# Optimization experiments

Hardware: AMD Instinct MI355X
Metric: run time of the kernel (lower is better)

Reference implementation:

```python
import jax, jax.numpy as jnp
import numpy as np
import math

EMBED_DIM = 1024
NUM_HEADS = 16
HEAD_DIM = EMBED_DIM // NUM_HEADS
ROPE_BASE = 10000.0


def _rope_cache(seq_len, dim, dtype=jnp.float32):
    inv_freq = 1.0 / (ROPE_BASE ** (jnp.arange(0, dim, 2, dtype=jnp.float32) / dim))
    t = jnp.arange(seq_len, dtype=jnp.float32)
    freqs = t[:, None] * inv_freq[None, :]          # [S, D/2]
    emb = jnp.concatenate([freqs, freqs], axis=-1)  # [S, D]
    return jnp.cos(emb).astype(dtype), jnp.sin(emb).astype(dtype)


def _rotate_half(x):
    x1, x2 = jnp.split(x, 2, axis=-1)
    return jnp.concatenate([-x2, x1], axis=-1)


def setup_inputs() -> dict:
    key = jax.random.key(0)
    ks = jax.random.split(key, 12)
    B, S, E = 2, 2048, EMBED_DIM
    s = 1.0 / math.sqrt(E)
    inp = {
        "query": jax.random.normal(ks[0], (B, S, E), jnp.float32),
        "key": jax.random.normal(ks[1], (B, S, E), jnp.float32),
        "value": jax.random.normal(ks[2], (B, S, E), jnp.float32),
        "Wq": jax.random.normal(ks[3], (E, E), jnp.float32) * s,
        "bq": jnp.zeros((E,), jnp.float32),
        "Wk": jax.random.normal(ks[4], (E, E), jnp.float32) * s,
        "bk": jnp.zeros((E,), jnp.float32),
        "Wv": jax.random.normal(ks[5], (E, E), jnp.float32) * s,
        "bv": jnp.zeros((E,), jnp.float32),
        "Wo": jax.random.normal(ks[6], (E, E), jnp.float32) * s,
        "bo": jnp.zeros((E,), jnp.float32),
    }
    return inp


def reference(query, key, value, Wq, bq, Wk, bk, Wv, bv, Wo, bo):
    B, S, E = query.shape
    H, D = NUM_HEADS, HEAD_DIM

    def proj(x, W, b):  # torch Linear: x @ W.T + b -> [B,H,S,D]
        return (x @ W.T + b).reshape(B, -1, H, D).transpose(0, 2, 1, 3)

    q = proj(query, Wq, bq)
    k = proj(key, Wk, bk)
    v = proj(value, Wv, bv)

    cos, sin = _rope_cache(S, D, q.dtype)  # [S, D]
    cos = cos[None, None]                  # [1,1,S,D]
    sin = sin[None, None]
    q = q * cos + _rotate_half(q) * sin
    k = k * cos + _rotate_half(k) * sin

    scale = 1.0 / math.sqrt(D)
    scores = jnp.einsum("bhsd,bhtd->bhst", q, k) * scale  # [B,H,S,S]
    causal = jnp.triu(jnp.ones((S, S), bool), k=1)
    scores = jnp.where(causal[None, None], -jnp.inf, scores)
    attn = jax.nn.softmax(scores, axis=-1)
    out = jnp.einsum("bhst,bhtd->bhsd", attn, v)           # [B,H,S,D]
    out = out.transpose(0, 2, 1, 3).reshape(B, S, E)
    return out @ Wo.T + bo
```

## Files before the change

kernel.cpp:

```cpp
#include <hip/hip_runtime.h>
#include <math.h>

typedef unsigned short u16;
typedef __attribute__((ext_vector_type(4))) float f32x4;
typedef __attribute__((ext_vector_type(8))) short bf16x8;

#define SEQ   2048
#define EMB   1024
#define NH    16
#define HD    64
#define MROWS 4096

__device__ __forceinline__ u16 f2b(float f) {
    unsigned u = __float_as_uint(f);
    u += 0x7fff + ((u >> 16) & 1);
    return (u16)(u >> 16);
}
__device__ __forceinline__ unsigned pack_bf16x2(float a, float b) {
    unsigned ua = __float_as_uint(a) + 0x8000u;
    unsigned ub = __float_as_uint(b) + 0x8000u;
    return __builtin_amdgcn_perm(ub, ua, 0x07060302u);
}
__device__ __forceinline__ void gld16(const u16* g, const u16* l) {
    __builtin_amdgcn_global_load_lds((const __attribute__((address_space(1))) void*)g,
                                     (__attribute__((address_space(3))) void*)l, 16, 0, 0);
}

__global__ void k_f2b3(const float* __restrict__ s0, const float* __restrict__ s1,
                       const float* __restrict__ s2, u16* d0, u16* d1, u16* d2, int n8) {
    const float* src = (blockIdx.z == 0) ? s0 : (blockIdx.z == 1 ? s1 : s2);
    u16* dst = (blockIdx.z == 0) ? d0 : (blockIdx.z == 1 ? d1 : d2);
    int i = blockIdx.x * blockDim.x + threadIdx.x;
    if (i >= n8) return;
    const float4* s4 = (const float4*)src;
    float4 a = s4[i * 2], b = s4[i * 2 + 1];
    union { u16 u[8]; uint4 v; } o;
    o.u[0] = f2b(a.x); o.u[1] = f2b(a.y); o.u[2] = f2b(a.z); o.u[3] = f2b(a.w);
    o.u[4] = f2b(b.x); o.u[5] = f2b(b.y); o.u[6] = f2b(b.z); o.u[7] = f2b(b.w);
    ((uint4*)dst)[i] = o.v;
}
__global__ void k_f2b4(const float* __restrict__ s0, const float* __restrict__ s1,
                       const float* __restrict__ s2, const float* __restrict__ s3,
                       u16* d0, u16* d1, u16* d2, u16* d3, int n8) {
    const float* src = (blockIdx.z == 0) ? s0 : (blockIdx.z == 1 ? s1 : (blockIdx.z == 2 ? s2 : s3));
    u16* dst = (blockIdx.z == 0) ? d0 : (blockIdx.z == 1 ? d1 : (blockIdx.z == 2 ? d2 : d3));
    int i = blockIdx.x * blockDim.x + threadIdx.x;
    if (i >= n8) return;
    const float4* s4 = (const float4*)src;
    float4 a = s4[i * 2], b = s4[i * 2 + 1];
    union { u16 u[8]; uint4 v; } o;
    o.u[0] = f2b(a.x); o.u[1] = f2b(a.y); o.u[2] = f2b(a.z); o.u[3] = f2b(a.w);
    o.u[4] = f2b(b.x); o.u[5] = f2b(b.y); o.u[6] = f2b(b.z); o.u[7] = f2b(b.w);
    ((uint4*)dst)[i] = o.v;
}

struct GemmArgs {
    const u16* A; const u16* Bw; const float* bias; u16* Cb; float* Cf;
};

__global__ __launch_bounds__(256) void k_gemm_bt(GemmArgs g0, GemmArgs g1, GemmArgs g2,
                                                 int K, int mode) {
    GemmArgs g = (blockIdx.z == 0) ? g0 : (blockIdx.z == 1 ? g1 : g2);
    __shared__ u16 sbuf[2][8192];

    int tid = threadIdx.x;
    int wave = tid >> 6, lane = tid & 63, quad = lane >> 4, l16 = lane & 15;
    int wm = wave >> 1, wn = wave & 1;
    int m0 = blockIdx.y * 128, n0 = blockIdx.x * 128;

    auto stage = [&](int k0, u16* buf) {
#pragma unroll
        for (int pp = 0; pp < 4; pp++) {
            int slot = pp * 256 + tid;
            int p = slot & 3;
            const u16* gsrc;
            if (pp < 2) {
                int row = slot >> 2;
                int c = p ^ (row & 3);
                gsrc = g.A + (size_t)(m0 + row) * K + k0 + c * 8;
            } else {
                int row = (slot >> 2) - 128;
                int c = p ^ (row & 3);
                gsrc = g.Bw + (size_t)(n0 + row) * K + k0 + c * 8;
            }
            gld16(gsrc, buf + slot * 8);
        }
    };

    f32x4 acc[4][4];
#pragma unroll
    for (int i = 0; i < 4; i++)
#pragma unroll
        for (int j = 0; j < 4; j++) acc[i][j] = (f32x4){0.f, 0.f, 0.f, 0.f};

    int nk = K >> 5;
    stage(0, sbuf[0]);
    for (int ks = 0; ks < nk; ks++) {
        __syncthreads();
        if (ks + 1 < nk) stage((ks + 1) << 5, sbuf[(ks + 1) & 1]);
        const u16* Ab = sbuf[ks & 1];
        const u16* Bb = Ab + 4096;
        bf16x8 af[4], bfr[4];
#pragma unroll
        for (int i = 0; i < 4; i++) {
            int row = wm * 64 + i * 16 + l16;
            af[i] = *(const bf16x8*)&Ab[row * 32 + (quad ^ (row & 3)) * 8];
        }
#pragma unroll
        for (int j = 0; j < 4; j++) {
            int row = wn * 64 + j * 16 + l16;
            bfr[j] = *(const bf16x8*)&Bb[row * 32 + (quad ^ (row & 3)) * 8];
        }
#pragma unroll
        for (int i = 0; i < 4; i++)
#pragma unroll
            for (int j = 0; j < 4; j++)
                acc[i][j] = __builtin_amdgcn_mfma_f32_16x16x32_bf16(af[i], bfr[j], acc[i][j], 0, 0, 0);
    }

    if (mode == 0) {
        if (blockIdx.z < 2) {
            float qscale = (blockIdx.z == 0) ? 0.18033688011112042f : 1.0f;
#pragma unroll
            for (int j = 0; j < 2; j++) {
                int col1 = n0 + wn * 64 + j * 16 + l16;
                int dd1 = col1 & 63;
                int h = col1 >> 6;
                float inv = __expf(-(float)dd1 * 0.28782313662425575f);
                float b1 = g.bias[col1], b2 = g.bias[col1 + 32];
#pragma unroll
                for (int i = 0; i < 4; i++)
#pragma unroll
                    for (int r = 0; r < 4; r++) {
                        int row = m0 + wm * 64 + i * 16 + quad * 4 + r;
                        int b = row >> 11, s = row & (SEQ - 1);
                        float sn, cs;
                        __sincosf((float)s * inv, &sn, &cs);
                        float x1 = acc[i][j][r] + b1;
                        float x2 = acc[i][j + 2][r] + b2;
                        size_t base = ((size_t)(b * NH + h) * SEQ + s) << 6;
                        g.Cb[base + dd1]      = f2b((x1 * cs - x2 * sn) * qscale);
                        g.Cb[base + dd1 + 32] = f2b((x2 * cs + x1 * sn) * qscale);
                    }
            }
        } else {
#pragma unroll
            for (int j = 0; j < 4; j++) {
                int col = n0 + wn * 64 + j * 16 + l16;
                float bv = g.bias[col];
                int h = col >> 6, dd = col & 63;
#pragma unroll
                for (int i = 0; i < 4; i++)
#pragma unroll
                    for (int r = 0; r < 4; r++) {
                        int row = m0 + wm * 64 + i * 16 + quad * 4 + r;
                        int b = row >> 11, s = row & (SEQ - 1);
                        g.Cb[((size_t)((b * NH + h) * HD) + dd) * SEQ + s] = f2b(acc[i][j][r] + bv);
                    }
            }
        }
    } else {
#pragma unroll
        for (int i = 0; i < 4; i++)
#pragma unroll
            for (int r = 0; r < 4; r++) {
                int row = m0 + wm * 64 + i * 16 + quad * 4 + r;
#pragma unroll
                for (int j = 0; j < 4; j++) {
                    int col = n0 + wn * 64 + j * 16 + l16;
                    g.Cf[(size_t)row * EMB + col] = acc[i][j][r] + g.bias[col];
                }
            }
    }
}

__global__ __launch_bounds__(256, 2) void k_attn(const u16* __restrict__ Q,
                                                 const u16* __restrict__ K,
                                                 const u16* __restrict__ Vt,
                                                 u16* __restrict__ O) {
    __shared__ u16 sbuf[2][8192];
    __shared__ u16 Pl[4][3072];
    int tid = threadIdx.x;
    int w = tid >> 6, lane = tid & 63, quad = lane >> 4, l16 = lane & 15;
    int bh = blockIdx.y;
    int qt = (blockIdx.y & 16) ? blockIdx.x : (15 - blockIdx.x);
    int q0w = qt * 128 + w * 32;

    const u16* Qb = Q + (size_t)bh * SEQ * HD;
    const u16* Kb = K + (size_t)bh * SEQ * HD;
    const u16* Vb = Vt + (size_t)bh * HD * SEQ;
    u16* pl = Pl[w];

    auto stage = [&](int t0, u16* buf) {
#pragma unroll
        for (int pp = 0; pp < 4; pp++) {
            int slot = pp * 256 + tid;
            int r = (slot >> 3) & 63;
            int p = slot & 7;
            int c = p ^ (r & 7);
            const u16* gsrc = (pp < 2) ? Kb + (size_t)(t0 + r) * HD + c * 8
                                       : Vb + (size_t)r * SEQ + t0 + c * 8;
            gld16(gsrc, buf + slot * 8);
        }
    };

    bf16x8 bq[2][2];
#pragma unroll
    for (int g = 0; g < 2; g++) {
        size_t base = (size_t)(q0w + g * 16 + l16) * HD + quad * 8;
        bq[g][0] = *(const bf16x8*)&Qb[base];
        bq[g][1] = *(const bf16x8*)&Qb[base + 32];
    }

    f32x4 o2[2][4];
#pragma unroll
    for (int g = 0; g < 2; g++)
#pragma unroll
        for (int jd = 0; jd < 4; jd++) o2[g][jd] = (f32x4){0.f, 0.f, 0.f, 0.f};
    float m_i[2] = {-INFINITY, -INFINITY};
    float l_p[2] = {0.f, 0.f};

    int niter = 2 * qt + 2;
    stage(0, sbuf[0]);
    for (int it = 0; it < niter; ++it) {
        __syncthreads();
        if (it + 1 < niter) stage((it + 1) * 64, sbuf[(it + 1) & 1]);
        const u16* Kl = sbuf[it & 1];
        const u16* Vl = Kl + 4096;
        int t0 = it * 64;

        bf16x8 kf[4][2], vf[4][2];
#pragma unroll
        for (int mt = 0; mt < 4; mt++) {
            int row = mt * 16 + l16;
            kf[mt][0] = *(const bf16x8*)&Kl[row * 64 + (quad ^ (row & 7)) * 8];
            kf[mt][1] = *(const bf16x8*)&Kl[row * 64 + ((quad + 4) ^ (row & 7)) * 8];
            vf[mt][0] = *(const bf16x8*)&Vl[row * 64 + (quad ^ (row & 7)) * 8];
            vf[mt][1] = *(const bf16x8*)&Vl[row * 64 + ((quad + 4) ^ (row & 7)) * 8];
        }

#pragma unroll
        for (int g = 0; g < 2; g++) {
            int qmin = q0w + g * 16;
            if (t0 > qmin + 15) continue;

            f32x4 sc[4];
#pragma unroll
            for (int mt = 0; mt < 4; mt++) {
                sc[mt] = (f32x4){0.f, 0.f, 0.f, 0.f};
                sc[mt] = __builtin_amdgcn_mfma_f32_16x16x32_bf16(kf[mt][0], bq[g][0], sc[mt], 0, 0, 0);
                sc[mt] = __builtin_amdgcn_mfma_f32_16x16x32_bf16(kf[mt][1], bq[g][1], sc[mt], 0, 0, 0);
            }

            if (t0 + 63 > qmin) {
                int q = qmin + l16;
#pragma unroll
                for (int mt = 0; mt < 4; mt++)
#pragma unroll
                    for (int r = 0; r < 4; r++) {
                        int t = t0 + mt * 16 + quad * 4 + r;
                        if (t > q) sc[mt][r] = -INFINITY;
                    }
            }

            float rm = -INFINITY;
#pragma unroll
            for (int mt = 0; mt < 4; mt++)
#pragma unroll
                for (int r = 0; r < 4; r++) rm = fmaxf(rm, sc[mt][r]);
            rm = fmaxf(rm, __shfl_xor(rm, 16, 64));
            rm = fmaxf(rm, __shfl_xor(rm, 32, 64));
            float mnew = fmaxf(m_i[g], rm);
            float al = __builtin_amdgcn_exp2f(m_i[g] - mnew);
            m_i[g] = mnew;

            float rs = 0.f;
#pragma unroll
            for (int mt = 0; mt < 4; mt++)
#pragma unroll
                for (int r = 0; r < 4; r++) {
                    float p = __builtin_amdgcn_exp2f(sc[mt][r] - mnew);
                    sc[mt][r] = p;
                    rs += p;
                }
            l_p[g] = l_p[g] * al + rs;

            u16* plg = pl + g * 1024;
#pragma unroll
            for (int mt = 0; mt < 4; mt++) {
                uint2 pk;
                pk.x = pack_bf16x2(sc[mt][0], sc[mt][1]);
                pk.y = pack_bf16x2(sc[mt][2], sc[mt][3]);
                int chunk = 2 * mt + (quad >> 1);
                *(uint2*)&plg[l16 * 64 + (chunk ^ (l16 & 7)) * 8 + (quad & 1) * 4] = pk;
            }

#pragma unroll
            for (int jd = 0; jd < 4; jd++)
#pragma unroll
                for (int r = 0; r < 4; r++) o2[g][jd][r] *= al;

            bf16x8 pb0 = *(const bf16x8*)&plg[l16 * 64 + (quad ^ (l16 & 7)) * 8];
            bf16x8 pb1 = *(const bf16x8*)&plg[l16 * 64 + ((quad + 4) ^ (l16 & 7)) * 8];

#pragma unroll
            for (int jd = 0; jd < 4; jd++) {
                o2[g][jd] = __builtin_amdgcn_mfma_f32_16x16x32_bf16(vf[jd][0], pb0, o2[g][jd], 0, 0, 0);
                o2[g][jd] = __builtin_amdgcn_mfma_f32_16x16x32_bf16(vf[jd][1], pb1, o2[g][jd], 0, 0, 0);
            }
        }
    }

    int b = bh >> 4, h = bh & (NH - 1);
#pragma unroll
    for (int g = 0; g < 2; g++) {
        float l = l_p[g];
        l += __shfl_xor(l, 16, 64);
        l += __shfl_xor(l, 32, 64);
        float inv = 1.f / l;
#pragma unroll
        for (int jd = 0; jd < 4; jd++) {
            uint2 pk;
            pk.x = pack_bf16x2(o2[g][jd][0] * inv, o2[g][jd][1] * inv);
            pk.y = pack_bf16x2(o2[g][jd][2] * inv, o2[g][jd][3] * inv);
            *(uint2*)&pl[l16 * 72 + jd * 16 + quad * 4] = pk;
        }
        int row = lane >> 2, dc = (lane & 3) * 16;
        uint4 d0 = *(const uint4*)&pl[row * 72 + dc];
        uint4 d1 = *(const uint4*)&pl[row * 72 + dc + 8];
        int q = q0w + g * 16 + row;
        size_t addr = (size_t)(b * SEQ + q) * EMB + h * HD + dc;
        *(uint4*)&O[addr] = d0;
        *(uint4*)&O[addr + 8] = d1;
    }
}

extern "C" void kernel_launch(void* const* d_in, const int* in_sizes, int n_in,
                              void* d_out, int out_size, void* d_ws, size_t ws_size,
                              hipStream_t stream) {
    const float* query = (const float*)d_in[0];
    const float* key_  = (const float*)d_in[1];
    const float* value = (const float*)d_in[2];
    const float* Wq = (const float*)d_in[3];
    const float* bq = (const float*)d_in[4];
    const float* Wk = (const float*)d_in[5];
    const float* bk = (const float*)d_in[6];
    const float* Wv = (const float*)d_in[7];
    const float* bv = (const float*)d_in[8];
    const float* Wo = (const float*)d_in[9];
    const float* bo = (const float*)d_in[10];
    float* out = (float*)d_out;

    char* ws = (char*)d_ws;
    const size_t MB = 1u << 20;
    u16* xq  = (u16*)(ws + 0 * MB);
    u16* xk  = (u16*)(ws + 8 * MB);
    u16* xv  = (u16*)(ws + 16 * MB);
    u16* wqb = (u16*)(ws + 24 * MB);
    u16* wkb = (u16*)(ws + 26 * MB);
    u16* wvb = (u16*)(ws + 28 * MB);
    u16* wob = (u16*)(ws + 30 * MB);
    u16* Qp  = (u16*)(ws + 32 * MB);
    u16* Kp  = (u16*)(ws + 40 * MB);
    u16* Vt  = (u16*)(ws + 48 * MB);
    u16* Ab  = xk;

    const int NX = MROWS * EMB;
    const int NW = EMB * EMB;

    k_f2b3<<<dim3(NX / (256 * 8), 1, 3), 256, 0, stream>>>(query, key_, value, xq, xk, xv, NX / 8);
    k_f2b4<<<dim3(NW / (256 * 8), 1, 4), 256, 0, stream>>>(Wq, Wk, Wv, Wo, wqb, wkb, wvb, wob, NW / 8);

    GemmArgs gq = { xq, wqb, bq, Qp, nullptr };
    GemmArgs gk = { xk, wkb, bk, Kp, nullptr };
    GemmArgs gv = { xv, wvb, bv, Vt, nullptr };
    k_gemm_bt<<<dim3(EMB / 128, MROWS / 128, 3), 256, 0, stream>>>(gq, gk, gv, EMB, 0);

    k_attn<<<dim3(16, 32), 256, 0, stream>>>(Qp, Kp, Vt, Ab);

    GemmArgs go = { Ab, wob, bo, nullptr, out };
    k_gemm_bt<<<dim3(EMB / 128, MROWS / 128, 1), 256, 0, stream>>>(go, go, go, EMB, 1);
}
```

Baseline: 242.5 us.

## Persistent attention scheduler, LDS-transposed V epilogue, smaller-tile output GEMM

Attention becomes a persistent kernel with 768 blocks that pull (head, query-tile) items from a global atomic counter, longest causal tiles first, for better load balance. The counter is zeroed by a new kernel and lives in the xv workspace buffer. The V projection epilogue now transposes through shared memory so it writes coalesced 16-byte stores instead of scattered 2-byte ones. The output projection gets its own 64x128-tile GEMM kernel to launch more blocks. Costs are an extra launch, an atomic per work item, and the loss of the launch_bounds occupancy hint on attention.

```diff
diff --git a/kernel.cpp b/kernel.cpp
--- a/kernel.cpp
+++ b/kernel.cpp
@@ -54,19 +54,24 @@
     ((uint4*)dst)[i] = o.v;
 }
 
+__global__ void k_zero(int* p) { if (threadIdx.x == 0) *p = 0; }
+
 struct GemmArgs {
-    const u16* A; const u16* Bw; const float* bias; u16* Cb; float* Cf;
+    const u16* A; const u16* Bw; const float* bias; u16* Cb;
 };
 
-__global__ __launch_bounds__(256) void k_gemm_bt(GemmArgs g0, GemmArgs g1, GemmArgs g2,
-                                                 int K, int mode) {
+__global__ __launch_bounds__(256) void k_gemm_qkv(GemmArgs g0, GemmArgs g1, GemmArgs g2) {
     GemmArgs g = (blockIdx.z == 0) ? g0 : (blockIdx.z == 1 ? g1 : g2);
-    __shared__ u16 sbuf[2][8192];
+    __shared__ union {
+        u16 s[2][8192];
+        u16 tr[4][4608];
+    } sh;
 
     int tid = threadIdx.x;
     int wave = tid >> 6, lane = tid & 63, quad = lane >> 4, l16 = lane & 15;
     int wm = wave >> 1, wn = wave & 1;
     int m0 = blockIdx.y * 128, n0 = blockIdx.x * 128;
+    const int K = EMB;
 
     auto stage = [&](int k0, u16* buf) {
 #pragma unroll
@@ -94,11 +99,11 @@
         for (int j = 0; j < 4; j++) acc[i][j] = (f32x4){0.f, 0.f, 0.f, 0.f};
 
     int nk = K >> 5;
-    stage(0, sbuf[0]);
+    stage(0, sh.s[0]);
     for (int ks = 0; ks < nk; ks++) {
         __syncthreads();
-        if (ks + 1 < nk) stage((ks + 1) << 5, sbuf[(ks + 1) & 1]);
-        const u16* Ab = sbuf[ks & 1];
+        if (ks + 1 < nk) stage((ks + 1) << 5, sh.s[(ks + 1) & 1]);
+        const u16* Ab = sh.s[ks & 1];
         const u16* Bb = Ab + 4096;
         bf16x8 af[4], bfr[4];
 #pragma unroll
@@ -118,220 +123,296 @@
                 acc[i][j] = __builtin_amdgcn_mfma_f32_16x16x32_bf16(af[i], bfr[j], acc[i][j], 0, 0, 0);
     }
 
-    if (mode == 0) {
-        if (blockIdx.z < 2) {
-            float qscale = (blockIdx.z == 0) ? 0.18033688011112042f : 1.0f;
-#pragma unroll
-            for (int j = 0; j < 2; j++) {
-                int col1 = n0 + wn * 64 + j * 16 + l16;
-                int dd1 = col1 & 63;
-                int h = col1 >> 6;
-                float inv = __expf(-(float)dd1 * 0.28782313662425575f);
-                float b1 = g.bias[col1], b2 = g.bias[col1 + 32];
-#pragma unroll
-                for (int i = 0; i < 4; i++)
-#pragma unroll
-                    for (int r = 0; r < 4; r++) {
-                        int row = m0 + wm * 64 + i * 16 + quad * 4 + r;
-                        int b = row >> 11, s = row & (SEQ - 1);
-                        float sn, cs;
-                        __sincosf((float)s * inv, &sn, &cs);
-                        float x1 = acc[i][j][r] + b1;
-                        float x2 = acc[i][j + 2][r] + b2;
-                        size_t base = ((size_t)(b * NH + h) * SEQ + s) << 6;
-                        g.Cb[base + dd1]      = f2b((x1 * cs - x2 * sn) * qscale);
-                        g.Cb[base + dd1 + 32] = f2b((x2 * cs + x1 * sn) * qscale);
-                    }
-            }
-        } else {
-#pragma unroll
-            for (int j = 0; j < 4; j++) {
-                int col = n0 + wn * 64 + j * 16 + l16;
-                float bv = g.bias[col];
-                int h = col >> 6, dd = col & 63;
-#pragma unroll
-                for (int i = 0; i < 4; i++)
-#pragma unroll
-                    for (int r = 0; r < 4; r++) {
-                        int row = m0 + wm * 64 + i * 16 + quad * 4 + r;
-                        int b = row >> 11, s = row & (SEQ - 1);
-                        g.Cb[((size_t)((b * NH + h) * HD) + dd) * SEQ + s] = f2b(acc[i][j][r] + bv);
-                    }
-            }
+    if (blockIdx.z < 2) {
+        float qscale = (blockIdx.z == 0) ? 0.18033688011112042f : 1.0f;
+#pragma unroll
+        for (int j = 0; j < 2; j++) {
+            int col1 = n0 + wn * 64 + j * 16 + l16;
+            int dd1 = col1 & 63;
+            int h = col1 >> 6;
+            float inv = __expf(-(float)dd1 * 0.28782313662425575f);
+            float b1 = g.bias[col1], b2 = g.bias[col1 + 32];
+#pragma unroll
+            for (int i = 0; i < 4; i++)
+#pragma unroll
+                for (int r = 0; r < 4; r++) {
+                    int row = m0 + wm * 64 + i * 16 + quad * 4 + r;
+                    int b = row >> 11, s = row & (SEQ - 1);
+                    float sn, cs;
+                    __sincosf((float)s * inv, &sn, &cs);
+                    float x1 = acc[i][j][r] + b1;
+                    float x2 = acc[i][j + 2][r] + b2;
+                    size_t base = ((size_t)(b * NH + h) * SEQ + s) << 6;
+                    g.Cb[base + dd1]      = f2b((x1 * cs - x2 * sn) * qscale);
+                    g.Cb[base + dd1 + 32] = f2b((x2 * cs + x1 * sn) * qscale);
+                }
         }
     } else {
-#pragma unroll
-        for (int i = 0; i < 4; i++)
-#pragma unroll
-            for (int r = 0; r < 4; r++) {
-                int row = m0 + wm * 64 + i * 16 + quad * 4 + r;
-#pragma unroll
-                for (int j = 0; j < 4; j++) {
-                    int col = n0 + wn * 64 + j * 16 + l16;
-                    g.Cf[(size_t)row * EMB + col] = acc[i][j][r] + g.bias[col];
-                }
-            }
+        __syncthreads();
+        u16* tr = sh.tr[wave];
+        int h = (n0 >> 6) + wn;
+        int b = m0 >> 11;
+        int s0 = (m0 & (SEQ - 1)) + wm * 64;
+#pragma unroll
+        for (int j = 0; j < 4; j++) {
+            float bv = g.bias[n0 + wn * 64 + j * 16 + l16];
+#pragma unroll
+            for (int i = 0; i < 4; i++) {
+                uint2 pk;
+                pk.x = pack_bf16x2(acc[i][j][0] + bv, acc[i][j][1] + bv);
+                pk.y = pack_bf16x2(acc[i][j][2] + bv, acc[i][j][3] + bv);
+                *(uint2*)&tr[(j * 16 + l16) * 72 + i * 16 + quad * 4] = pk;
+            }
+        }
+        u16* dst = g.Cb + (((size_t)(b * NH + h) * HD) * SEQ) + s0;
+#pragma unroll
+        for (int ps = 0; ps < 8; ps++) {
+            int d = ps * 8 + (lane >> 3);
+            int sl = (lane & 7) * 8;
+            uint4 v = *(const uint4*)&tr[d * 72 + sl];
+            *(uint4*)&dst[(size_t)d * SEQ + sl] = v;
+        }
     }
 }
 
-__global__ __launch_bounds__(256, 2) void k_attn(const u16* __restrict__ Q,
-                                                 const u16* __restrict__ K,
-                                                 const u16* __restrict__ Vt,
-                                                 u16* __restrict__ O) {
-    __shared__ u16 sbuf[2][8192];
-    __shared__ u16 Pl[4][3072];
+__global__ __launch_bounds__(256) void k_gemm_o(const u16* __restrict__ A,
+                                                const u16* __restrict__ Bw,
+                                                const float* __restrict__ bias,
+                                                float* __restrict__ C) {
+    __shared__ u16 sb[2][6144];
     int tid = threadIdx.x;
     int w = tid >> 6, lane = tid & 63, quad = lane >> 4, l16 = lane & 15;
-    int bh = blockIdx.y;
-    int qt = (blockIdx.y & 16) ? blockIdx.x : (15 - blockIdx.x);
-    int q0w = qt * 128 + w * 32;
-
-    const u16* Qb = Q + (size_t)bh * SEQ * HD;
-    const u16* Kb = K + (size_t)bh * SEQ * HD;
-    const u16* Vb = Vt + (size_t)bh * HD * SEQ;
-    u16* pl = Pl[w];
-
-    auto stage = [&](int t0, u16* buf) {
-#pragma unroll
-        for (int pp = 0; pp < 4; pp++) {
+    int m0 = blockIdx.y * 64, n0 = blockIdx.x * 128;
+    const int K = EMB;
+
+    auto stage = [&](int k0, u16* buf) {
+#pragma unroll
+        for (int pp = 0; pp < 3; pp++) {
             int slot = pp * 256 + tid;
-            int r = (slot >> 3) & 63;
-            int p = slot & 7;
-            int c = p ^ (r & 7);
-            const u16* gsrc = (pp < 2) ? Kb + (size_t)(t0 + r) * HD + c * 8
-                                       : Vb + (size_t)r * SEQ + t0 + c * 8;
-            gld16(gsrc, buf + slot * 8);
+            if (slot < 256) {
+                int row = slot >> 2, p = slot & 3;
+                int c = p ^ (row & 3);
+                gld16(A + (size_t)(m0 + row) * K + k0 + c * 8, buf + slot * 8);
+            } else {
+                int s2 = slot - 256;
+                int row = s2 >> 2, p = s2 & 3;
+                int c = p ^ (row & 3);
+                gld16(Bw + (size_t)(n0 + row) * K + k0 + c * 8, buf + 2048 + s2 * 8);
+            }
         }
     };
 
-    bf16x8 bq[2][2];
-#pragma unroll
-    for (int g = 0; g < 2; g++) {
-        size_t base = (size_t)(q0w + g * 16 + l16) * HD + quad * 8;
-        bq[g][0] = *(const bf16x8*)&Qb[base];
-        bq[g][1] = *(const bf16x8*)&Qb[base + 32];
+    f32x4 acc[4][2];
+#pragma unroll
+    for (int i = 0; i < 4; i++)
+#pragma unroll
+        for (int j = 0; j < 2; j++) acc[i][j] = (f32x4){0.f, 0.f, 0.f, 0.f};
+
+    int nk = K >> 5;
+    stage(0, sb[0]);
+    for (int ks = 0; ks < nk; ks++) {
+        __syncthreads();
+        if (ks + 1 < nk) stage((ks + 1) << 5, sb[(ks + 1) & 1]);
+        const u16* Ab = sb[ks & 1];
+        const u16* Bb = Ab + 2048;
+        bf16x8 af[4], bf[2];
+#pragma unroll
+        for (int i = 0; i < 4; i++) {
+            int row = i * 16 + l16;
+            af[i] = *(const bf16x8*)&Ab[row * 32 + (quad ^ (row & 3)) * 8];
+        }
+#pragma unroll
+        for (int j = 0; j < 2; j++) {
+            int row = w * 32 + j * 16 + l16;
+            bf[j] = *(const bf16x8*)&Bb[row * 32 + (quad ^ (row & 3)) * 8];
+        }
+#pragma unroll
+        for (int i = 0; i < 4; i++)
+#pragma unroll
+            for (int j = 0; j < 2; j++)
+                acc[i][j] = __builtin_amdgcn_mfma_f32_16x16x32_bf16(af[i], bf[j], acc[i][j], 0, 0, 0);
     }
 
-    f32x4 o2[2][4];
-#pragma unroll
-    for (int g = 0; g < 2; g++)
-#pragma unroll
-        for (int jd = 0; jd < 4; jd++) o2[g][jd] = (f32x4){0.f, 0.f, 0.f, 0.f};
-    float m_i[2] = {-INFINITY, -INFINITY};
-    float l_p[2] = {0.f, 0.f};
-
-    int niter = 2 * qt + 2;
-    stage(0, sbuf[0]);
-    for (int it = 0; it < niter; ++it) {
+#pragma unroll
+    for (int i = 0; i < 4; i++)
+#pragma unroll
+        for (int r = 0; r < 4; r++) {
+            int row = m0 + i * 16 + quad * 4 + r;
+#pragma unroll
+            for (int j = 0; j < 2; j++) {
+                int col = n0 + w * 32 + j * 16 + l16;
+                C[(size_t)row * EMB + col] = acc[i][j][r] + bias[col];
+            }
+        }
+}
+
+__global__ __launch_bounds__(256) void k_attn(const u16* __restrict__ Q,
+                                              const u16* __restrict__ K,
+                                              const u16* __restrict__ Vt,
+                                              u16* __restrict__ O,
+                                              int* __restrict__ ctr) {
+    __shared__ u16 sbuf[2][8192];
+    __shared__ u16 Pl[4][2048];
+    __shared__ int item_s;
+    int tid = threadIdx.x;
+    int w = tid >> 6, lane = tid & 63, quad = lane >> 4, l16 = lane & 15;
+
+    for (;;) {
+        if (tid == 0) item_s = atomicAdd(ctr, 1);
         __syncthreads();
-        if (it + 1 < niter) stage((it + 1) * 64, sbuf[(it + 1) & 1]);
-        const u16* Kl = sbuf[it & 1];
-        const u16* Vl = Kl + 4096;
-        int t0 = it * 64;
-
-        bf16x8 kf[4][2], vf[4][2];
-#pragma unroll
-        for (int mt = 0; mt < 4; mt++) {
-            int row = mt * 16 + l16;
-            kf[mt][0] = *(const bf16x8*)&Kl[row * 64 + (quad ^ (row & 7)) * 8];
-            kf[mt][1] = *(const bf16x8*)&Kl[row * 64 + ((quad + 4) ^ (row & 7)) * 8];
-            vf[mt][0] = *(const bf16x8*)&Vl[row * 64 + (quad ^ (row & 7)) * 8];
-            vf[mt][1] = *(const bf16x8*)&Vl[row * 64 + ((quad + 4) ^ (row & 7)) * 8];
-        }
-
+        int item = item_s;
+        if (item >= 512) return;
+        int bh = item & 31;
+        int qt = 15 - (item >> 5);
+        int q0w = qt * 128 + w * 32;
+
+        const u16* Qb = Q + (size_t)bh * SEQ * HD;
+        const u16* Kb = K + (size_t)bh * SEQ * HD;
+        const u16* Vb = Vt + (size_t)bh * HD * SEQ;
+        u16* pl = Pl[w];
+
+        bf16x8 bq[2][2];
 #pragma unroll
         for (int g = 0; g < 2; g++) {
-            int qmin = q0w + g * 16;
-            if (t0 > qmin + 15) continue;
-
-            f32x4 sc[4];
+            size_t base = (size_t)(q0w + g * 16 + l16) * HD + quad * 8;
+            bq[g][0] = *(const bf16x8*)&Qb[base];
+            bq[g][1] = *(const bf16x8*)&Qb[base + 32];
+        }
+
+        f32x4 o2[2][4];
+#pragma unroll
+        for (int g = 0; g < 2; g++)
+#pragma unroll
+            for (int jd = 0; jd < 4; jd++) o2[g][jd] = (f32x4){0.f, 0.f, 0.f, 0.f};
+        float m_i[2] = {-INFINITY, -INFINITY};
+        float l_p[2] = {0.f, 0.f};
+
+        auto stage = [&](int t0, u16* buf) {
+#pragma unroll
+            for (int pp = 0; pp < 4; pp++) {
+                int slot = pp * 256 + tid;
+                int r = (slot >> 3) & 63;
+                int p = slot & 7;
+                int c = p ^ (r & 7);
+                const u16* gsrc = (pp < 2) ? Kb + (size_t)(t0 + r) * HD + c * 8
+                                           : Vb + (size_t)r * SEQ + t0 + c * 8;
+                gld16(gsrc, buf + slot * 8);
+            }
+        };
+
+        int niter = 2 * qt + 2;
+        stage(0, sbuf[0]);
+        for (int it = 0; it < niter; ++it) {
+            __syncthreads();
+            if (it + 1 < niter) stage((it + 1) * 64, sbuf[(it + 1) & 1]);
+            const u16* Kl = sbuf[it & 1];
+            const u16* Vl = Kl + 4096;
+            int t0 = it * 64;
+
+            bf16x8 kf[4][2], vf[4][2];
 #pragma unroll
             for (int mt = 0; mt < 4; mt++) {
-                sc[mt] = (f32x4){0.f, 0.f, 0.f, 0.f};
-                sc[mt] = __builtin_amdgcn_mfma_f32_16x16x32_bf16(kf[mt][0], bq[g][0], sc[mt], 0, 0, 0);
-                sc[mt] = __builtin_amdgcn_mfma_f32_16x16x32_bf16(kf[mt][1], bq[g][1], sc[mt], 0, 0, 0);
-            }
-
-            if (t0 + 63 > qmin) {
-                int q = qmin + l16;
+                int row = mt * 16 + l16;
+                kf[mt][0] = *(const bf16x8*)&Kl[row * 64 + (quad ^ (row & 7)) * 8];
+                kf[mt][1] = *(const bf16x8*)&Kl[row * 64 + ((quad + 4) ^ (row & 7)) * 8];
+                vf[mt][0] = *(const bf16x8*)&Vl[row * 64 + (quad ^ (row & 7)) * 8];
+                vf[mt][1] = *(const bf16x8*)&Vl[row * 64 + ((quad + 4) ^ (row & 7)) * 8];
+            }
+
+#pragma unroll
+            for (int g = 0; g < 2; g++) {
+                int qmin = q0w + g * 16;
+                if (t0 > qmin + 15) continue;
+
+                f32x4 sc[4];
+#pragma unroll
+                for (int mt = 0; mt < 4; mt++) {
+                    sc[mt] = (f32x4){0.f, 0.f, 0.f, 0.f};
+                    sc[mt] = __builtin_amdgcn_mfma_f32_16x16x32_bf16(kf[mt][0], bq[g][0], sc[mt], 0, 0, 0);
+                    sc[mt] = __builtin_amdgcn_mfma_f32_16x16x32_bf16(kf[mt][1], bq[g][1], sc[mt], 0, 0, 0);
+                }
+
+                if (t0 + 63 > qmin) {
+                    int q = qmin + l16;
+#pragma unroll
+                    for (int mt = 0; mt < 4; mt++)
+#pragma unroll
+                        for (int r = 0; r < 4; r++) {
+                            int t = t0 + mt * 16 + quad * 4 + r;
+                            if (t > q) sc[mt][r] = -INFINITY;
+                        }
+                }
+
+                float rm = -INFINITY;
 #pragma unroll
                 for (int mt = 0; mt < 4; mt++)
 #pragma unroll
+                    for (int r = 0; r < 4; r++) rm = fmaxf(rm, sc[mt][r]);
+                rm = fmaxf(rm, __shfl_xor(rm, 16, 64));
+                rm = fmaxf(rm, __shfl_xor(rm, 32, 64));
+                float mnew = fmaxf(m_i[g], rm);
+                float al = __builtin_amdgcn_exp2f(m_i[g] - mnew);
+                m_i[g] = mnew;
+
+                float rs = 0.f;
+#pragma unroll
+                for (int mt = 0; mt < 4; mt++)
+#pragma unroll
                     for (int r = 0; r < 4; r++) {
-                        int t = t0 + mt * 16 + quad * 4 + r;
-                        if (t > q) sc[mt][r] = -INFINITY;
+                        float p = __builtin_amdgcn_exp2f(sc[mt][r] - mnew);
+                        sc[mt][r] = p;
+                        rs += p;
                     }
-            }
-
-            float rm = -INFINITY;
-#pragma unroll
-            for (int mt = 0; mt < 4; mt++)
-#pragma unroll
-                for (int r = 0; r < 4; r++) rm = fmaxf(rm, sc[mt][r]);
-            rm = fmaxf(rm, __shfl_xor(rm, 16, 64));
-            rm = fmaxf(rm, __shfl_xor(rm, 32, 64));
-            float mnew = fmaxf(m_i[g], rm);
-            float al = __builtin_amdgcn_exp2f(m_i[g] - mnew);
-            m_i[g] = mnew;
-
-            float rs = 0.f;
-#pragma unroll
-            for (int mt = 0; mt < 4; mt++)
-#pragma unroll
-                for (int r = 0; r < 4; r++) {
-                    float p = __builtin_amdgcn_exp2f(sc[mt][r] - mnew);
-                    sc[mt][r] = p;
-                    rs += p;
+                l_p[g] = l_p[g] * al + rs;
+
+                u16* plg = pl + g * 1024;
+#pragma unroll
+                for (int mt = 0; mt < 4; mt++) {
+                    uint2 pk;
+                    pk.x = pack_bf16x2(sc[mt][0], sc[mt][1]);
+                    pk.y = pack_bf16x2(sc[mt][2], sc[mt][3]);
+                    int chunk = 2 * mt + (quad >> 1);
+                    *(uint2*)&plg[l16 * 64 + (chunk ^ (l16 & 7)) * 8 + (quad & 1) * 4] = pk;
                 }
-            l_p[g] = l_p[g] * al + rs;
-
-            u16* plg = pl + g * 1024;
-#pragma unroll
-            for (int mt = 0; mt < 4; mt++) {
+
+#pragma unroll
+                for (int jd = 0; jd < 4; jd++)
+#pragma unroll
+                    for (int r = 0; r < 4; r++) o2[g][jd][r] *= al;
+
+                bf16x8 pb0 = *(const bf16x8*)&plg[l16 * 64 + (quad ^ (l16 & 7)) * 8];
+                bf16x8 pb1 = *(const bf16x8*)&plg[l16 * 64 + ((quad + 4) ^ (l16 & 7)) * 8];
+
+#pragma unroll
+                for (int jd = 0; jd < 4; jd++) {
+                    o2[g][jd] = __builtin_amdgcn_mfma_f32_16x16x32_bf16(vf[jd][0], pb0, o2[g][jd], 0, 0, 0);
+                    o2[g][jd] = __builtin_amdgcn_mfma_f32_16x16x32_bf16(vf[jd][1], pb1, o2[g][jd], 0, 0, 0);
+                }
+            }
+        }
+
+        int b = bh >> 4, h = bh & (NH - 1);
+#pragma unroll
+        for (int g = 0; g < 2; g++) {
+            float l = l_p[g];
+            l += __shfl_xor(l, 16, 64);
+            l += __shfl_xor(l, 32, 64);
+            float inv = 1.f / l;
+#pragma unroll
+            for (int jd = 0; jd < 4; jd++) {
                 uint2 pk;
-                pk.x = pack_bf16x2(sc[mt][0], sc[mt][1]);
-                pk.y = pack_bf16x2(sc[mt][2], sc[mt][3]);
-                int chunk = 2 * mt + (quad >> 1);
-                *(uint2*)&plg[l16 * 64 + (chunk ^ (l16 & 7)) * 8 + (quad & 1) * 4] = pk;
-            }
-
-#pragma unroll
-            for (int jd = 0; jd < 4; jd++)
-#pragma unroll
-                for (int r = 0; r < 4; r++) o2[g][jd][r] *= al;
-
-            bf16x8 pb0 = *(const bf16x8*)&plg[l16 * 64 + (quad ^ (l16 & 7)) * 8];
-            bf16x8 pb1 = *(const bf16x8*)&plg[l16 * 64 + ((quad + 4) ^ (l16 & 7)) * 8];
-
-#pragma unroll
-            for (int jd = 0; jd < 4; jd++) {
-                o2[g][jd] = __builtin_amdgcn_mfma_f32_16x16x32_bf16(vf[jd][0], pb0, o2[g][jd], 0, 0, 0);
-                o2[g][jd] = __builtin_amdgcn_mfma_f32_16x16x32_bf16(vf[jd][1], pb1, o2[g][jd], 0, 0, 0);
-            }
-        }
-    }
-
-    int b = bh >> 4, h = bh & (NH - 1);
-#pragma unroll
-    for (int g = 0; g < 2; g++) {
-        float l = l_p[g];
-        l += __shfl_xor(l, 16, 64);
-        l += __shfl_xor(l, 32, 64);
-        float inv = 1.f / l;
-#pragma unroll
-        for (int jd = 0; jd < 4; jd++) {
-            uint2 pk;
-            pk.x = pack_bf16x2(o2[g][jd][0] * inv, o2[g][jd][1] * inv);
-            pk.y = pack_bf16x2(o2[g][jd][2] * inv, o2[g][jd][3] * inv);
-            *(uint2*)&pl[l16 * 72 + jd * 16 + quad * 4] = pk;
-        }
-        int row = lane >> 2, dc = (lane & 3) * 16;
-        uint4 d0 = *(const uint4*)&pl[row * 72 + dc];
-        uint4 d1 = *(const uint4*)&pl[row * 72 + dc + 8];
-        int q = q0w + g * 16 + row;
-        size_t addr = (size_t)(b * SEQ + q) * EMB + h * HD + dc;
-        *(uint4*)&O[addr] = d0;
-        *(uint4*)&O[addr + 8] = d1;
+                pk.x = pack_bf16x2(o2[g][jd][0] * inv, o2[g][jd][1] * inv);
+                pk.y = pack_bf16x2(o2[g][jd][2] * inv, o2[g][jd][3] * inv);
+                *(uint2*)&pl[l16 * 72 + jd * 16 + quad * 4] = pk;
+            }
+            int row = lane >> 2, dc = (lane & 3) * 16;
+            uint4 d0 = *(const uint4*)&pl[row * 72 + dc];
+            uint4 d1 = *(const uint4*)&pl[row * 72 + dc + 8];
+            int q = q0w + g * 16 + row;
+            size_t addr = (size_t)(b * SEQ + q) * EMB + h * HD + dc;
+            *(uint4*)&O[addr] = d0;
+            *(uint4*)&O[addr + 8] = d1;
+        }
     }
 }
 
@@ -364,6 +445,7 @@
     u16* Kp  = (u16*)(ws + 40 * MB);
     u16* Vt  = (u16*)(ws + 48 * MB);
     u16* Ab  = xk;
+    int* ctr = (int*)xv;
 
     const int NX = MROWS * EMB;
     const int NW = EMB * EMB;
@@ -371,13 +453,13 @@
     k_f2b3<<<dim3(NX / (256 * 8), 1, 3), 256, 0, stream>>>(query, key_, value, xq, xk, xv, NX / 8);
     k_f2b4<<<dim3(NW / (256 * 8), 1, 4), 256, 0, stream>>>(Wq, Wk, Wv, Wo, wqb, wkb, wvb, wob, NW / 8);
 
-    GemmArgs gq = { xq, wqb, bq, Qp, nullptr };
-    GemmArgs gk = { xk, wkb, bk, Kp, nullptr };
-    GemmArgs gv = { xv, wvb, bv, Vt, nullptr };
-    k_gemm_bt<<<dim3(EMB / 128, MROWS / 128, 3), 256, 0, stream>>>(gq, gk, gv, EMB, 0);
-
-    k_attn<<<dim3(16, 32), 256, 0, stream>>>(Qp, Kp, Vt, Ab);
-
-    GemmArgs go = { Ab, wob, bo, nullptr, out };
-    k_gemm_bt<<<dim3(EMB / 128, MROWS / 128, 1), 256, 0, stream>>>(go, go, go, EMB, 1);
-}
+    GemmArgs gq = { xq, wqb, bq, Qp };
+    GemmArgs gk = { xk, wkb, bk, Kp };
+    GemmArgs gv = { xv, wvb, bv, Vt };
+    k_gemm_qkv<<<dim3(EMB / 128, MROWS / 128, 3), 256, 0, stream>>>(gq, gk, gv);
+
+    k_zero<<<1, 64, 0, stream>>>(ctr);
+    k_attn<<<768, 256, 0, stream>>>(Qp, Kp, Vt, Ab, ctr);
+
+    k_gemm_o<<<dim3(EMB / 128, MROWS / 64), 256, 0, stream>>>(Ab, wob, bo, out);
+}
```

New measurement: 245.1 us. No clear change (+1.1%).
